# Kernel tuning notes

Measured on AMD Instinct MI355X. Metric: run time of the kernel, lower is better.

## Reference

```python
import jax, jax.numpy as jnp
import numpy as np

BETA = 0.25

def setup_inputs() -> dict:
    key = jax.random.key(0)
    k1, k2 = jax.random.split(key)
    x = jax.random.normal(k1, (32, 32, 32, 64), dtype=jnp.float32)
    # tf.random_uniform_initializer default: uniform in [-0.05, 0.05]
    embeddings = jax.random.uniform(k2, (64, 1024), dtype=jnp.float32,
                                    minval=-0.05, maxval=0.05)
    return {"x": x, "embeddings": embeddings}

def reference(x, embeddings):
    D, K = embeddings.shape
    flat = x.reshape(-1, D)                                   # [N, D]
    # squared L2 distances to each codebook vector (expanded form)
    sim = flat @ embeddings                                   # [N, K]
    dists = (jnp.sum(flat * flat, axis=1, keepdims=True)
             + jnp.sum(embeddings * embeddings, axis=0)
             - 2.0 * sim)                                     # [N, K]
    idx = jnp.argmin(dists, axis=1)                           # [N]
    quantized = embeddings.T[idx].reshape(x.shape)            # gather == one-hot matmul
    commitment_loss = BETA * jnp.mean((jax.lax.stop_gradient(quantized) - x) ** 2)
    codebook_loss = jnp.mean((quantized - jax.lax.stop_gradient(x)) ** 2)
    loss = commitment_loss + codebook_loss
    out = x + jax.lax.stop_gradient(quantized - x)            # straight-through
    return out, loss
```

## Files before the change

kernel.cpp:

```cpp
#include <hip/hip_runtime.h>
#include <hip/hip_bf16.h>


#define NROWS 32768
#define DDIM  64
#define KCODE 1024
#define NELEM (NROWS * DDIM)
#define MARGIN 4e-3f
#define FIXBLOCKS 256
#define MAINBLK 256

typedef __attribute__((ext_vector_type(8))) _Float16 f16x8;
typedef __attribute__((ext_vector_type(4))) float f32x4;

static __device__ __forceinline__ unsigned short f2h(float v) {
    _Float16 h = (_Float16)v;
    unsigned short b;
    __builtin_memcpy(&b, &h, 2);
    return b;
}
static __device__ __forceinline__ void gload16(const void* g, void* l) {
    __builtin_amdgcn_global_load_lds(
        (const __attribute__((address_space(1))) void*)g,
        (__attribute__((address_space(3))) void*)l, 16, 0, 0);
}

__global__ void vq_prep(const float* __restrict__ e,
                        float* __restrict__ se,
                        float* __restrict__ eT,
                        unsigned short* __restrict__ ehSw,
                        int* __restrict__ ctrl) {
    __shared__ float tile[64][17];
    const int t = threadIdx.x;
    const int k0 = blockIdx.x * 16;
    if (blockIdx.x == 0 && t < 4) ctrl[t] = 0;
    #pragma unroll
    for (int i = 0; i < 4; ++i) {
        int idx = i * 256 + t;
        int d = idx >> 4, kk = idx & 15;
        tile[d][kk] = e[d * KCODE + k0 + kk];
    }
    __syncthreads();
    if (t < 16) {
        float s = 0.f;
        #pragma unroll
        for (int d = 0; d < 64; ++d) { float v = tile[d][t]; s = fmaf(v, v, s); }
        se[k0 + t] = s;
    }
    const int kk = t >> 4;
    const int dg = (t & 15) * 4;
    const int kg = k0 + kk;
    float v0 = tile[dg + 0][kk], v1 = tile[dg + 1][kk];
    float v2 = tile[dg + 2][kk], v3 = tile[dg + 3][kk];
    *(float4*)&eT[(size_t)kg * 64 + dg] = make_float4(v0, v1, v2, v3);
    const int sw = (((dg >> 3) ^ (kg & 7)) << 3) + (dg & 7);
    *(ushort4*)&ehSw[(size_t)kg * 64 + sw] =
        make_ushort4(f2h(v0), f2h(v1), f2h(v2), f2h(v3));
}

__launch_bounds__(512)
__global__ void vq_main(const float* __restrict__ x,
                        const float* __restrict__ se,
                        const float* __restrict__ eT,
                        const unsigned short* __restrict__ ehSw,
                        float* __restrict__ out,
                        float* __restrict__ parts,
                        int* __restrict__ cnt,
                        int2* __restrict__ list) {
    __shared__ unsigned short Beh[KCODE * 64];
    __shared__ float sse[KCODE];
    __shared__ float wsum[8];

    const int t = threadIdx.x;
    const int lane = t & 63;
    const int w = t >> 6;
    const int quad = lane >> 4, l15 = lane & 15;
    const int rowBase = blockIdx.x * 128 + w * 16;

    {
        const unsigned char* g = (const unsigned char*)ehSw;
        #pragma unroll
        for (int r = 0; r < 16; ++r)
            gload16(g + (size_t)(r * 512 + t) * 16, &Beh[(r * 512 + t) * 8]);
        float2 s2 = ((const float2*)se)[t];
        sse[2 * t + 0] = s2.x;
        sse[2 * t + 1] = s2.y;
    }

    f16x8 ah0, ah1, al0, al1;
    {
        const float4* ap0 = (const float4*)(x + (size_t)(rowBase + l15) * 64 + quad * 8);
        const float4* ap1 = (const float4*)(x + (size_t)(rowBase + l15) * 64 + 32 + quad * 8);
        float4 a0 = ap0[0], a1 = ap0[1], b0 = ap1[0], b1 = ap1[1];
        float av[8] = {a0.x, a0.y, a0.z, a0.w, a1.x, a1.y, a1.z, a1.w};
        float bv[8] = {b0.x, b0.y, b0.z, b0.w, b1.x, b1.y, b1.z, b1.w};
        f16x8 h0, h1, l0, l1;
        #pragma unroll
        for (int j = 0; j < 8; ++j) {
            _Float16 ha = (_Float16)av[j];
            _Float16 hb = (_Float16)bv[j];
            h0[j] = ha;
            h1[j] = hb;
            l0[j] = (_Float16)(av[j] - (float)ha);
            l1[j] = (_Float16)(bv[j] - (float)hb);
        }
        ah0 = h0; ah1 = h1; al0 = l0; al1 = l1;
    }
    __syncthreads();

    float sb[4], sb2[4];
    int   si[4];
    #pragma unroll
    for (int r = 0; r < 4; ++r) { sb[r] = 3.4e38f; sb2[r] = 3.4e38f; si[r] = 0; }

    const int slot0 = ((quad ^ (l15 & 7)) << 3);
    const int slot1 = (((quad + 4) ^ (l15 & 7)) << 3);

    #pragma unroll 4
    for (int nt = 0; nt < 64; ++nt) {
        const int code = nt * 16 + l15;
        f16x8 b0 = *(const f16x8*)&Beh[code * 64 + slot0];
        f16x8 b1 = *(const f16x8*)&Beh[code * 64 + slot1];
        float cse = sse[code];
        f32x4 aA = {0.f, 0.f, 0.f, 0.f}, aB = {0.f, 0.f, 0.f, 0.f};
        aA = __builtin_amdgcn_mfma_f32_16x16x32_f16(ah0, b0, aA, 0, 0, 0);
        aB = __builtin_amdgcn_mfma_f32_16x16x32_f16(ah1, b1, aB, 0, 0, 0);
        aA = __builtin_amdgcn_mfma_f32_16x16x32_f16(al0, b0, aA, 0, 0, 0);
        aB = __builtin_amdgcn_mfma_f32_16x16x32_f16(al1, b1, aB, 0, 0, 0);
        #pragma unroll
        for (int r = 0; r < 4; ++r) {
            float key = fmaf(-2.f, aA[r] + aB[r], cse);
            bool lt = key < sb[r];
            sb2[r] = fminf(sb2[r], fmaxf(sb[r], key));
            sb[r]  = fminf(sb[r], key);
            si[r]  = lt ? code : si[r];
        }
    }

    #pragma unroll
    for (int m = 1; m < 16; m <<= 1) {
        #pragma unroll
        for (int r = 0; r < 4; ++r) {
            float ob  = __shfl_xor(sb[r],  m, 64);
            float ob2 = __shfl_xor(sb2[r], m, 64);
            int   oi  = __shfl_xor(si[r],  m, 64);
            float nb2 = fminf(fminf(sb2[r], ob2), fmaxf(sb[r], ob));
            bool take = (ob < sb[r]) || (ob == sb[r] && oi < si[r]);
            sb[r] = take ? ob : sb[r];
            si[r] = take ? oi : si[r];
            sb2[r] = nb2;
        }
    }

    if (l15 == 0) {
        #pragma unroll
        for (int r = 0; r < 4; ++r) {
            if (sb2[r] - sb[r] < MARGIN) {
                int p = atomicAdd(cnt, 1);
                list[p] = make_int2(rowBase + quad * 4 + r, si[r]);
            }
        }
    }

    int src = (l15 >> 2) << 4;
    int j0 = __shfl(si[0], src, 64);
    int j1 = __shfl(si[1], src, 64);
    int j2 = __shfl(si[2], src, 64);
    int j3 = __shfl(si[3], src, 64);
    int rsel = l15 & 3;
    int myidx = rsel == 0 ? j0 : (rsel == 1 ? j1 : (rsel == 2 ? j2 : j3));

    {
        const float4* qrow = (const float4*)(eT + (size_t)myidx * 64 + quad * 16);
        const float4* xrow = (const float4*)(x + (size_t)(rowBase + l15) * 64 + quad * 16);
        float4* orow = (float4*)(out + (size_t)(rowBase + l15) * 64 + quad * 16);
        float lsum = 0.f;
        #pragma unroll
        for (int i = 0; i < 4; ++i) {
            float4 q = qrow[i];
            float4 xv = xrow[i];
            float4 o;
            float dx;
            dx = q.x - xv.x; o.x = xv.x + dx; lsum = fmaf(dx, dx, lsum);
            dx = q.y - xv.y; o.y = xv.y + dx; lsum = fmaf(dx, dx, lsum);
            dx = q.z - xv.z; o.z = xv.z + dx; lsum = fmaf(dx, dx, lsum);
            dx = q.w - xv.w; o.w = xv.w + dx; lsum = fmaf(dx, dx, lsum);
            orow[i] = o;
        }
        #pragma unroll
        for (int off = 32; off > 0; off >>= 1)
            lsum += __shfl_down(lsum, off, 64);
        if (lane == 0) wsum[w] = lsum;
    }
    __syncthreads();
    if (t == 0) {
        float s = 0.f;
        #pragma unroll
        for (int i = 0; i < 8; ++i) s += wsum[i];
        parts[blockIdx.x] = s;
    }
}

__launch_bounds__(256)
__global__ void vq_fix(const float* __restrict__ x,
                       const float* __restrict__ se,
                       const float* __restrict__ eT,
                       const int2* __restrict__ list,
                       const int* __restrict__ cnt,
                       const float* __restrict__ parts,
                       float* __restrict__ lossAcc,
                       int* __restrict__ done,
                       float* __restrict__ out) {
    __shared__ float xs[64];
    __shared__ float cb[256];
    __shared__ int   ci[256];
    __shared__ int   newIdxS;
    __shared__ int   lastS;
    const int t = threadIdx.x;
    const int n = *cnt;

    for (int i = blockIdx.x; i < n; i += gridDim.x) {
        int2 en = list[i];
        const int row = en.x, oldIdx = en.y;
        if (t < 64) xs[t] = x[(size_t)row * 64 + t];
        __syncthreads();

        float sx = 0.f;
        #pragma unroll
        for (int d = 0; d < 64; ++d) sx = fmaf(xs[d], xs[d], sx);

        const int k0 = t * 4;
        const float4* e0 = (const float4*)(eT + (size_t)(k0 + 0) * 64);
        const float4* e1 = (const float4*)(eT + (size_t)(k0 + 1) * 64);
        const float4* e2 = (const float4*)(eT + (size_t)(k0 + 2) * 64);
        const float4* e3 = (const float4*)(eT + (size_t)(k0 + 3) * 64);
        float dot0 = 0.f, dot1 = 0.f, dot2 = 0.f, dot3 = 0.f;
        #pragma unroll
        for (int i4 = 0; i4 < 16; ++i4) {
            float4 v0 = e0[i4], v1 = e1[i4], v2 = e2[i4], v3 = e3[i4];
            float xa = xs[4 * i4 + 0], xb = xs[4 * i4 + 1];
            float xc = xs[4 * i4 + 2], xd = xs[4 * i4 + 3];
            dot0 = fmaf(xa, v0.x, dot0); dot0 = fmaf(xb, v0.y, dot0);
            dot0 = fmaf(xc, v0.z, dot0); dot0 = fmaf(xd, v0.w, dot0);
            dot1 = fmaf(xa, v1.x, dot1); dot1 = fmaf(xb, v1.y, dot1);
            dot1 = fmaf(xc, v1.z, dot1); dot1 = fmaf(xd, v1.w, dot1);
            dot2 = fmaf(xa, v2.x, dot2); dot2 = fmaf(xb, v2.y, dot2);
            dot2 = fmaf(xc, v2.z, dot2); dot2 = fmaf(xd, v2.w, dot2);
            dot3 = fmaf(xa, v3.x, dot3); dot3 = fmaf(xb, v3.y, dot3);
            dot3 = fmaf(xc, v3.z, dot3); dot3 = fmaf(xd, v3.w, dot3);
        }
        float dd0 = (sx + se[k0 + 0]) - 2.0f * dot0;
        float dd1 = (sx + se[k0 + 1]) - 2.0f * dot1;
        float dd2 = (sx + se[k0 + 2]) - 2.0f * dot2;
        float dd3 = (sx + se[k0 + 3]) - 2.0f * dot3;
        float db = dd0; int di = k0;
        if (dd1 < db) { db = dd1; di = k0 + 1; }
        if (dd2 < db) { db = dd2; di = k0 + 2; }
        if (dd3 < db) { db = dd3; di = k0 + 3; }
        cb[t] = db; ci[t] = di;
        __syncthreads();

        if (t < 64) {
            float B = cb[t]; int I = ci[t];
            #pragma unroll
            for (int s = 64; s < 256; s += 64) {
                float b = cb[t + s]; int i2 = ci[t + s];
                bool take = (b < B) || (b == B && i2 < I);
                B = take ? b : B;
                I = take ? i2 : I;
            }
            #pragma unroll
            for (int m = 1; m < 64; m <<= 1) {
                float ob = __shfl_xor(B, m, 64);
                int   oi = __shfl_xor(I, m, 64);
                bool take = (ob < B) || (ob == B && oi < I);
                B = take ? ob : B;
                I = take ? oi : I;
            }
            if (t == 0) newIdxS = I;
        }
        __syncthreads();

        const int ni = newIdxS;
        if (ni != oldIdx) {
            if (t < 64) {
                float xv = xs[t];
                float qn = eT[(size_t)ni * 64 + t];
                float qo = eT[(size_t)oldIdx * 64 + t];
                float dn = qn - xv, dl = qo - xv;
                out[(size_t)row * 64 + t] = xv + dn;
                float delta = dn * dn - dl * dl;
                #pragma unroll
                for (int off = 32; off > 0; off >>= 1)
                    delta += __shfl_down(delta, off, 64);
                if (t == 0) atomicAdd(lossAcc, delta);
            }
        }
        __syncthreads();
    }

    if (t == 0) {
        __threadfence();
        int fin = atomicAdd(done, 1);
        lastS = (fin == FIXBLOCKS - 1) ? 1 : 0;
    }
    __syncthreads();
    if (lastS) {
        cb[t] = parts[t];
        __syncthreads();
        if (t < 64) {
            float v = cb[t] + cb[t + 64] + cb[t + 128] + cb[t + 192];
            #pragma unroll
            for (int off = 32; off > 0; off >>= 1)
                v += __shfl_down(v, off, 64);
            if (t == 0) {
                float total = v + atomicAdd(lossAcc, 0.0f);
                float m = total / (float)NELEM;
                out[NELEM] = 0.25f * m + m;
            }
        }
    }
}

extern "C" void kernel_launch(void* const* d_in, const int* in_sizes, int n_in,
                              void* d_out, int out_size, void* d_ws, size_t ws_size,
                              hipStream_t stream) {
    const float* x = (const float*)d_in[0];
    const float* e = (const float*)d_in[1];
    float* out = (float*)d_out;
    float* ws  = (float*)d_ws;

    float* lossAcc       = ws;
    int*   cnt           = (int*)(ws + 1);
    int*   done          = (int*)(ws + 2);
    float* se            = ws + 64;
    float* eT            = ws + 1280;
    unsigned short* ehSw = (unsigned short*)(ws + 66816);
    int2*  list          = (int2*)(ws + 99584);
    float* parts         = ws + 165120;

    vq_prep<<<64, 256, 0, stream>>>(e, se, eT, ehSw, (int*)ws);
    vq_main<<<MAINBLK, 512, 0, stream>>>(x, se, eT, ehSw, out, parts, cnt, list);
    vq_fix<<<FIXBLOCKS, 256, 0, stream>>>(x, se, eT, list, cnt, parts, lossAcc, done, out);
}
```

Measured before the change: 109.2 us.

## Fuse near-tie argmin recheck into main kernel and finalize loss in last block

```diff
diff --git a/kernel.cpp b/kernel.cpp
--- a/kernel.cpp
+++ b/kernel.cpp
@@ -7,7 +7,6 @@
 #define KCODE 1024
 #define NELEM (NROWS * DDIM)
 #define MARGIN 4e-3f
-#define FIXBLOCKS 256
 #define MAINBLK 256
 
 typedef __attribute__((ext_vector_type(8))) _Float16 f16x8;
@@ -65,17 +64,25 @@
                         const unsigned short* __restrict__ ehSw,
                         float* __restrict__ out,
                         float* __restrict__ parts,
-                        int* __restrict__ cnt,
-                        int2* __restrict__ list) {
+                        int* __restrict__ done) {
     __shared__ unsigned short Beh[KCODE * 64];
     __shared__ float sse[KCODE];
     __shared__ float wsum[8];
+    __shared__ float xs[64];
+    __shared__ float cb[512];
+    __shared__ int   ci[512];
+    __shared__ int   flagRows[128];
+    __shared__ int   idxRow[128];
+    __shared__ int   sNf;
+    __shared__ int   lastS;
 
     const int t = threadIdx.x;
     const int lane = t & 63;
     const int w = t >> 6;
     const int quad = lane >> 4, l15 = lane & 15;
     const int rowBase = blockIdx.x * 128 + w * 16;
+
+    if (t == 0) { sNf = 0; }
 
     {
         const unsigned char* g = (const unsigned char*)ehSw;
@@ -155,21 +162,71 @@
     if (l15 == 0) {
         #pragma unroll
         for (int r = 0; r < 4; ++r) {
+            const int rloc = w * 16 + quad * 4 + r;
+            idxRow[rloc] = si[r];
             if (sb2[r] - sb[r] < MARGIN) {
-                int p = atomicAdd(cnt, 1);
-                list[p] = make_int2(rowBase + quad * 4 + r, si[r]);
-            }
-        }
-    }
-
-    int src = (l15 >> 2) << 4;
-    int j0 = __shfl(si[0], src, 64);
-    int j1 = __shfl(si[1], src, 64);
-    int j2 = __shfl(si[2], src, 64);
-    int j3 = __shfl(si[3], src, 64);
-    int rsel = l15 & 3;
-    int myidx = rsel == 0 ? j0 : (rsel == 1 ? j1 : (rsel == 2 ? j2 : j3));
-
+                int p = atomicAdd(&sNf, 1);
+                flagRows[p] = rloc;
+            }
+        }
+    }
+    __syncthreads();
+
+    const int nf = sNf;
+    for (int i = 0; i < nf; ++i) {
+        const int rloc = flagRows[i];
+        const size_t grow = (size_t)blockIdx.x * 128 + rloc;
+        if (t < 64) xs[t] = x[grow * 64 + t];
+        __syncthreads();
+
+        float sx = 0.f;
+        #pragma unroll
+        for (int d = 0; d < 64; ++d) sx = fmaf(xs[d], xs[d], sx);
+
+        const int k0 = t * 2;
+        const float4* e0 = (const float4*)(eT + (size_t)(k0 + 0) * 64);
+        const float4* e1 = (const float4*)(eT + (size_t)(k0 + 1) * 64);
+        float dot0 = 0.f, dot1 = 0.f;
+        #pragma unroll
+        for (int i4 = 0; i4 < 16; ++i4) {
+            float4 v0 = e0[i4], v1 = e1[i4];
+            float xa = xs[4 * i4 + 0], xb = xs[4 * i4 + 1];
+            float xc = xs[4 * i4 + 2], xd = xs[4 * i4 + 3];
+            dot0 = fmaf(xa, v0.x, dot0); dot0 = fmaf(xb, v0.y, dot0);
+            dot0 = fmaf(xc, v0.z, dot0); dot0 = fmaf(xd, v0.w, dot0);
+            dot1 = fmaf(xa, v1.x, dot1); dot1 = fmaf(xb, v1.y, dot1);
+            dot1 = fmaf(xc, v1.z, dot1); dot1 = fmaf(xd, v1.w, dot1);
+        }
+        float dd0 = (sx + sse[k0 + 0]) - 2.0f * dot0;
+        float dd1 = (sx + sse[k0 + 1]) - 2.0f * dot1;
+        float db = dd0; int di = k0;
+        if (dd1 < db) { db = dd1; di = k0 + 1; }
+        cb[t] = db; ci[t] = di;
+        __syncthreads();
+
+        if (t < 64) {
+            float B = cb[t]; int I = ci[t];
+            #pragma unroll
+            for (int s = 64; s < 512; s += 64) {
+                float b = cb[t + s]; int i2 = ci[t + s];
+                bool take = (b < B) || (b == B && i2 < I);
+                B = take ? b : B;
+                I = take ? i2 : I;
+            }
+            #pragma unroll
+            for (int m = 1; m < 64; m <<= 1) {
+                float ob = __shfl_xor(B, m, 64);
+                int   oi = __shfl_xor(I, m, 64);
+                bool take = (ob < B) || (ob == B && oi < I);
+                B = take ? ob : B;
+                I = take ? oi : I;
+            }
+            if (t == 0) idxRow[rloc] = I;
+        }
+        __syncthreads();
+    }
+
+    const int myidx = idxRow[w * 16 + l15];
     {
         const float4* qrow = (const float4*)(eT + (size_t)myidx * 64 + quad * 16);
         const float4* xrow = (const float4*)(x + (size_t)(rowBase + l15) * 64 + quad * 16);
@@ -193,120 +250,22 @@
         if (lane == 0) wsum[w] = lsum;
     }
     __syncthreads();
+
     if (t == 0) {
         float s = 0.f;
         #pragma unroll
         for (int i = 0; i < 8; ++i) s += wsum[i];
-        parts[blockIdx.x] = s;
-    }
-}
-
-__launch_bounds__(256)
-__global__ void vq_fix(const float* __restrict__ x,
-                       const float* __restrict__ se,
-                       const float* __restrict__ eT,
-                       const int2* __restrict__ list,
-                       const int* __restrict__ cnt,
-                       const float* __restrict__ parts,
-                       float* __restrict__ lossAcc,
-                       int* __restrict__ done,
-                       float* __restrict__ out) {
-    __shared__ float xs[64];
-    __shared__ float cb[256];
-    __shared__ int   ci[256];
-    __shared__ int   newIdxS;
-    __shared__ int   lastS;
-    const int t = threadIdx.x;
-    const int n = *cnt;
-
-    for (int i = blockIdx.x; i < n; i += gridDim.x) {
-        int2 en = list[i];
-        const int row = en.x, oldIdx = en.y;
-        if (t < 64) xs[t] = x[(size_t)row * 64 + t];
-        __syncthreads();
-
-        float sx = 0.f;
-        #pragma unroll
-        for (int d = 0; d < 64; ++d) sx = fmaf(xs[d], xs[d], sx);
-
-        const int k0 = t * 4;
-        const float4* e0 = (const float4*)(eT + (size_t)(k0 + 0) * 64);
-        const float4* e1 = (const float4*)(eT + (size_t)(k0 + 1) * 64);
-        const float4* e2 = (const float4*)(eT + (size_t)(k0 + 2) * 64);
-        const float4* e3 = (const float4*)(eT + (size_t)(k0 + 3) * 64);
-        float dot0 = 0.f, dot1 = 0.f, dot2 = 0.f, dot3 = 0.f;
-        #pragma unroll
-        for (int i4 = 0; i4 < 16; ++i4) {
-            float4 v0 = e0[i4], v1 = e1[i4], v2 = e2[i4], v3 = e3[i4];
-            float xa = xs[4 * i4 + 0], xb = xs[4 * i4 + 1];
-            float xc = xs[4 * i4 + 2], xd = xs[4 * i4 + 3];
-            dot0 = fmaf(xa, v0.x, dot0); dot0 = fmaf(xb, v0.y, dot0);
-            dot0 = fmaf(xc, v0.z, dot0); dot0 = fmaf(xd, v0.w, dot0);
-            dot1 = fmaf(xa, v1.x, dot1); dot1 = fmaf(xb, v1.y, dot1);
-            dot1 = fmaf(xc, v1.z, dot1); dot1 = fmaf(xd, v1.w, dot1);
-            dot2 = fmaf(xa, v2.x, dot2); dot2 = fmaf(xb, v2.y, dot2);
-            dot2 = fmaf(xc, v2.z, dot2); dot2 = fmaf(xd, v2.w, dot2);
-            dot3 = fmaf(xa, v3.x, dot3); dot3 = fmaf(xb, v3.y, dot3);
-            dot3 = fmaf(xc, v3.z, dot3); dot3 = fmaf(xd, v3.w, dot3);
-        }
-        float dd0 = (sx + se[k0 + 0]) - 2.0f * dot0;
-        float dd1 = (sx + se[k0 + 1]) - 2.0f * dot1;
-        float dd2 = (sx + se[k0 + 2]) - 2.0f * dot2;
-        float dd3 = (sx + se[k0 + 3]) - 2.0f * dot3;
-        float db = dd0; int di = k0;
-        if (dd1 < db) { db = dd1; di = k0 + 1; }
-        if (dd2 < db) { db = dd2; di = k0 + 2; }
-        if (dd3 < db) { db = dd3; di = k0 + 3; }
-        cb[t] = db; ci[t] = di;
-        __syncthreads();
-
-        if (t < 64) {
-            float B = cb[t]; int I = ci[t];
-            #pragma unroll
-            for (int s = 64; s < 256; s += 64) {
-                float b = cb[t + s]; int i2 = ci[t + s];
-                bool take = (b < B) || (b == B && i2 < I);
-                B = take ? b : B;
-                I = take ? i2 : I;
-            }
-            #pragma unroll
-            for (int m = 1; m < 64; m <<= 1) {
-                float ob = __shfl_xor(B, m, 64);
-                int   oi = __shfl_xor(I, m, 64);
-                bool take = (ob < B) || (ob == B && oi < I);
-                B = take ? ob : B;
-                I = take ? oi : I;
-            }
-            if (t == 0) newIdxS = I;
-        }
-        __syncthreads();
-
-        const int ni = newIdxS;
-        if (ni != oldIdx) {
-            if (t < 64) {
-                float xv = xs[t];
-                float qn = eT[(size_t)ni * 64 + t];
-                float qo = eT[(size_t)oldIdx * 64 + t];
-                float dn = qn - xv, dl = qo - xv;
-                out[(size_t)row * 64 + t] = xv + dn;
-                float delta = dn * dn - dl * dl;
-                #pragma unroll
-                for (int off = 32; off > 0; off >>= 1)
-                    delta += __shfl_down(delta, off, 64);
-                if (t == 0) atomicAdd(lossAcc, delta);
-            }
-        }
-        __syncthreads();
-    }
-
-    if (t == 0) {
-        __threadfence();
-        int fin = atomicAdd(done, 1);
-        lastS = (fin == FIXBLOCKS - 1) ? 1 : 0;
+        __hip_atomic_store(&parts[blockIdx.x], s, __ATOMIC_RELEASE,
+                           __HIP_MEMORY_SCOPE_AGENT);
+        int fin = __hip_atomic_fetch_add(done, 1, __ATOMIC_ACQ_REL,
+                                         __HIP_MEMORY_SCOPE_AGENT);
+        lastS = (fin == MAINBLK - 1) ? 1 : 0;
     }
     __syncthreads();
     if (lastS) {
-        cb[t] = parts[t];
+        if (t < 256)
+            cb[t] = __hip_atomic_load(&parts[t], __ATOMIC_ACQUIRE,
+                                      __HIP_MEMORY_SCOPE_AGENT);
         __syncthreads();
         if (t < 64) {
             float v = cb[t] + cb[t + 64] + cb[t + 128] + cb[t + 192];
@@ -314,8 +273,7 @@
             for (int off = 32; off > 0; off >>= 1)
                 v += __shfl_down(v, off, 64);
             if (t == 0) {
-                float total = v + atomicAdd(lossAcc, 0.0f);
-                float m = total / (float)NELEM;
+                float m = v / (float)NELEM;
                 out[NELEM] = 0.25f * m + m;
             }
         }
@@ -330,16 +288,12 @@
     float* out = (float*)d_out;
     float* ws  = (float*)d_ws;
 
-    float* lossAcc       = ws;
-    int*   cnt           = (int*)(ws + 1);
     int*   done          = (int*)(ws + 2);
     float* se            = ws + 64;
     float* eT            = ws + 1280;
     unsigned short* ehSw = (unsigned short*)(ws + 66816);
-    int2*  list          = (int2*)(ws + 99584);
     float* parts         = ws + 165120;
 
     vq_prep<<<64, 256, 0, stream>>>(e, se, eT, ehSw, (int*)ws);
-    vq_main<<<MAINBLK, 512, 0, stream>>>(x, se, eT, ehSw, out, parts, cnt, list);
-    vq_fix<<<FIXBLOCKS, 256, 0, stream>>>(x, se, eT, list, cnt, parts, lossAcc, done, out);
-}
+    vq_main<<<MAINBLK, 512, 0, stream>>>(x, se, eT, ehSw, out, parts, done);
+}
```

New measurement: 113.8 us. 1.04x slower.
